# Kernel optimization log

Measured on AMD Instinct MI355X. Metric: run time of the kernel, lower is better.

Reference implementation:

```python
import jax, jax.numpy as jnp
import numpy as np


def setup_inputs() -> dict:
    key = jax.random.key(0)
    k1, k2, k3, k4 = jax.random.split(key, 4)
    B, T, C, H, W = 16, 8, 1024, 14, 14
    x = jax.random.normal(k1, (B * T, C, H, W), dtype=jnp.float32)
    # learned spectral filter, stored as real/imag pairs: [T, H, W, C//2+1, 2]
    wfilt = jax.random.normal(k2, (T, H, W, C // 2 + 1, 2), dtype=jnp.float32) * 0.02
    # 1x1x1 Conv3d over channels -> plain [out, in] matrix + bias
    conv_w = jax.random.normal(k3, (C, C), dtype=jnp.float32) * (1.0 / np.sqrt(C))
    conv_b = jax.random.normal(k4, (C,), dtype=jnp.float32) * 0.01
    return {"x": x, "wfilt": wfilt, "conv_w": conv_w, "conv_b": conv_b, "n_segments": T}


def reference(x, wfilt, conv_w, conv_b, n_segments):
    bt, c, h, w = x.shape
    t = n_segments
    b = bt // t
    x5 = x.reshape(b, t, c, h, w)
    # move channels last: [b, t, h, w, c]
    d = jnp.transpose(x5, (0, 1, 3, 4, 2))
    # rFFT along channel axis, ortho norm
    f = jnp.fft.rfft(d, axis=4, norm="ortho")  # [b, t, h, w, c//2+1]
    wc = jax.lax.complex(wfilt[..., 0], wfilt[..., 1])  # [t, h, w, c//2+1]
    f = f * wc  # broadcast over batch
    d = jnp.fft.irfft(f, n=c, axis=4, norm="ortho")  # [b, t, h, w, c]
    d = jnp.transpose(d, (0, 1, 4, 2, 3))  # [b, t, c, h, w]
    # enhancement: 1x1x1 Conv3d over channels + exact GELU
    e = jnp.einsum("btchw,oc->btohw", d, conv_w) + conv_b[None, None, :, None, None]
    e = jax.nn.gelu(e, approximate=False)
    return (x5 + e).reshape(bt, c, h, w)
```

## Files before the change

### kernel.cpp

```cpp
#include <hip/hip_runtime.h>
#include <hip/hip_bf16.h>
#include <math.h>

typedef short short8 __attribute__((ext_vector_type(8)));
typedef float f32x4 __attribute__((ext_vector_type(4)));

#define BTN   128
#define HWN   196
#define CCH   1024
#define NPIX  (BTN * HWN)
#define BTSTR (CCH * HWN)

#define WS_D  0
#define WS_BW 51380224

__device__ __forceinline__ float2 cadd(float2 a, float2 b) { return make_float2(a.x + b.x, a.y + b.y); }
__device__ __forceinline__ float2 csub(float2 a, float2 b) { return make_float2(a.x - b.x, a.y - b.y); }
__device__ __forceinline__ float2 cmulf(float2 a, float2 b) {
  return make_float2(a.x * b.x - a.y * b.y, a.x * b.y + a.y * b.x);
}
__device__ __forceinline__ float2 cmulc(float2 a, float2 b) {
  return make_float2(a.x * b.x + a.y * b.y, a.y * b.x - a.x * b.y);
}
__device__ __forceinline__ float2 csqr(float2 a) {
  return make_float2(a.x * a.x - a.y * a.y, 2.f * a.x * a.y);
}
__device__ __forceinline__ float2 cneg(float2 a) { return make_float2(-a.x, -a.y); }
__device__ __forceinline__ unsigned short f2bf(float f) {
  unsigned u = __float_as_uint(f);
  unsigned r = (u + 0x7fffu + ((u >> 16) & 1u)) >> 16;
  return (unsigned short)r;
}

__global__ void wcast_kernel(const float* __restrict__ w, unsigned short* __restrict__ o) {
  int i = (blockIdx.x * 256 + threadIdx.x) * 4;
  float4 v = *(const float4*)(w + i);
  uint2 u;
  u.x = (unsigned)f2bf(v.x) | ((unsigned)f2bf(v.y) << 16);
  u.y = (unsigned)f2bf(v.z) | ((unsigned)f2bf(v.w) << 16);
  *(uint2*)(o + i) = u;
}

#define TS 1028

__global__ __launch_bounds__(256) void fft_filter_kernel(
    const float* __restrict__ x, const float* __restrict__ wfilt,
    unsigned short* __restrict__ dmat) {
  __shared__ float tile[8 * TS];
  __shared__ float2 tw10s[257];
  int tid = threadIdx.x;
  int l = tid & 63, w = tid >> 6;

  for (int i = tid; i < 257; i += 256) {
    float s, c;
    __sincosf(-6.283185307179586f * (float)i / 1024.0f, &s, &c);
    tw10s[i] = make_float2(c, s);
  }

  int blk = (blockIdx.x & 7) * 392 + (blockIdx.x >> 3);
  int p_base = blk * 8;

  {
    int g = tid & 1, chb = tid >> 1;
    int p = p_base + 4 * g;
    int bt = p / HWN, hw = p - bt * HWN;
    const float* src = x + (size_t)bt * BTSTR + hw;
    float* rowb = tile + (4 * g) * TS;
#pragma unroll
    for (int it = 0; it < 8; ++it) {
      int c = chb + 128 * it;
      float4 v = *(const float4*)(src + (size_t)c * HWN);
      float* b = rowb + c;
      b[0 * TS] = v.x; b[1 * TS] = v.y; b[2 * TS] = v.z; b[3 * TS] = v.w;
    }
  }
  __syncthreads();

  const float H = 0.70710678118654752f;
  float2 Wl;
  { float s, c; __sincosf(-6.283185307179586f * (float)l / 512.0f, &s, &c); Wl = make_float2(c, s); }
  float2 W2l = csqr(Wl), W4l = csqr(W2l);
  float2 W2li = make_float2(W2l.y, -W2l.x);
  float2 T01 = cmulf(Wl, make_float2(H, -H));
  float2 T02 = make_float2(Wl.y, -Wl.x);
  float2 T03 = cmulf(Wl, make_float2(-H, -H));
  float2 t3 = csqr(W4l); if (l & 32) t3 = cneg(t3);
  float2 t4 = csqr(t3);  if (l & 16) t4 = cneg(t4);
  float2 t5 = csqr(t4);  if (l & 8)  t5 = cneg(t5);
  float2 t6 = csqr(t5);  if (l & 4)  t6 = cneg(t6);
  float2 t7 = csqr(t6);  if (l & 2)  t7 = cneg(t7);

#pragma unroll 1
  for (int pp = 0; pp < 2; ++pp) {
    int px = w * 2 + pp;
    int p = p_base + px;
    int bt = p / HWN, hw = p - bt * HWN;
    float2* zrow = (float2*)(tile + px * TS);

    float2 zr[8];
#pragma unroll
    for (int r = 0; r < 8; ++r) zr[r] = zrow[l + 64 * r];

    {
      float2 T0[4] = {Wl, T01, T02, T03};
#pragma unroll
      for (int r = 0; r < 4; ++r) {
        float2 a = zr[r], b = zr[r + 4];
        zr[r] = cadd(a, b);
        zr[r + 4] = cmulf(csub(a, b), T0[r]);
      }
    }
#pragma unroll
    for (int h = 0; h < 2; ++h) {
      int b0 = h * 4;
      float2 a = zr[b0], b = zr[b0 + 2];
      zr[b0] = cadd(a, b); zr[b0 + 2] = cmulf(csub(a, b), W2l);
      a = zr[b0 + 1]; b = zr[b0 + 3];
      zr[b0 + 1] = cadd(a, b); zr[b0 + 3] = cmulf(csub(a, b), W2li);
    }
#pragma unroll
    for (int r = 0; r < 8; r += 2) {
      float2 a = zr[r], b = zr[r + 1];
      zr[r] = cadd(a, b); zr[r + 1] = cmulf(csub(a, b), W4l);
    }
    {
      float2 tws[6] = {t3, t4, t5, t6, t7, make_float2(1.f, 0.f)};
      int masks[6] = {32, 16, 8, 4, 2, 1};
#pragma unroll
      for (int s = 0; s < 6; ++s) {
        int m = masks[s];
        bool up = (l & m) != 0;
        float2 te = up ? tws[s] : make_float2(1.f, 0.f);
#pragma unroll
        for (int r = 0; r < 8; ++r) {
          float2 v = zr[r];
          float2 o = make_float2(__shfl_xor(v.x, m, 64), __shfl_xor(v.y, m, 64));
          float2 d = up ? csub(o, v) : cadd(v, o);
          zr[r] = cmulf(d, te);
        }
      }
    }

#pragma unroll
    for (int r = 0; r < 8; ++r) zrow[l + 64 * r] = zr[r];
    {
      float2* z = zrow;
      const float* wf = wfilt + (size_t)((bt & 7) * HWN + hw) * 1026;
      const float sc = 1.0f / 512.0f;
#pragma unroll
      for (int i = 0; i < 4; ++i) {
        int f = 64 * i + l;
        if (f == 0) {
          float2 z0 = z[0];
          float X0 = z0.x + z0.y, X512 = z0.x - z0.y;
          float Y0 = X0 * wf[0] * sc;
          float Y512 = X512 * wf[1024] * sc;
          z[0] = make_float2(0.5f * (Y0 + Y512), 0.5f * (Y0 - Y512));
          float2 z2 = z[1];
          float2 X256 = make_float2(z2.x, -z2.y);
          float2 Y = cmulf(X256, make_float2(wf[512], wf[513]));
          z[1] = make_float2(Y.x * sc, -Y.y * sc);
        } else {
          int g = 512 - f;
          int pf = (int)(__brev((unsigned)f) >> 23);
          int pg = (int)(__brev((unsigned)g) >> 23);
          float2 Zf = z[pf], Zg = z[pg];
          float2 A = make_float2(0.5f * (Zf.x + Zg.x), 0.5f * (Zf.y - Zg.y));
          float2 B = make_float2(0.5f * (Zf.y + Zg.y), -0.5f * (Zf.x - Zg.x));
          float2 Wf = tw10s[f];
          float2 WB = cmulf(Wf, B);
          float2 Xf = make_float2(A.x + WB.x, A.y + WB.y);
          float2 Xg = make_float2(A.x - WB.x, -(A.y - WB.y));
          float2 Yf = cmulf(Xf, make_float2(wf[2 * f], wf[2 * f + 1]));
          float2 Yg = cmulf(Xg, make_float2(wf[2 * g], wf[2 * g + 1]));
          Yf.x *= sc; Yf.y *= sc; Yg.x *= sc; Yg.y *= sc;
          float2 Ap = make_float2(0.5f * (Yf.x + Yg.x), 0.5f * (Yf.y - Yg.y));
          float2 T  = make_float2(0.5f * (Yf.x - Yg.x), 0.5f * (Yf.y + Yg.y));
          float2 Bp = cmulf(make_float2(Wf.x, -Wf.y), T);
          z[pf] = make_float2(Ap.x - Bp.y, Ap.y + Bp.x);
          z[pg] = make_float2(Ap.x + Bp.y, Bp.x - Ap.y);
        }
      }
    }
#pragma unroll
    for (int r = 0; r < 8; ++r) zr[r] = zrow[l + 64 * r];

    {
      float2 tws[6] = {make_float2(1.f, 0.f), t7, t6, t5, t4, t3};
      int masks[6] = {1, 2, 4, 8, 16, 32};
#pragma unroll
      for (int s = 0; s < 6; ++s) {
        int m = masks[s];
        bool up = (l & m) != 0;
        float2 te = up ? make_float2(tws[s].x, -tws[s].y) : make_float2(1.f, 0.f);
#pragma unroll
        for (int r = 0; r < 8; ++r) {
          float2 v = cmulf(zr[r], te);
          float2 o = make_float2(__shfl_xor(v.x, m, 64), __shfl_xor(v.y, m, 64));
          zr[r] = up ? csub(o, v) : cadd(v, o);
        }
      }
    }
#pragma unroll
    for (int r = 0; r < 8; r += 2) {
      float2 v = cmulc(zr[r + 1], W4l);
      float2 a = zr[r];
      zr[r] = cadd(a, v); zr[r + 1] = csub(a, v);
    }
#pragma unroll
    for (int h = 0; h < 2; ++h) {
      int b0 = h * 4;
      float2 v = cmulc(zr[b0 + 2], W2l);
      float2 a = zr[b0];
      zr[b0] = cadd(a, v); zr[b0 + 2] = csub(a, v);
      v = cmulc(zr[b0 + 3], W2li);
      a = zr[b0 + 1];
      zr[b0 + 1] = cadd(a, v); zr[b0 + 3] = csub(a, v);
    }
    {
      float2 T0[4] = {Wl, T01, T02, T03};
#pragma unroll
      for (int r = 0; r < 4; ++r) {
        float2 v = cmulc(zr[r + 4], T0[r]);
        float2 a = zr[r];
        zr[r] = cadd(a, v); zr[r + 4] = csub(a, v);
      }
    }

    unsigned* dst = (unsigned*)(dmat + (size_t)p * CCH);
#pragma unroll
    for (int r = 0; r < 8; ++r) {
      float2 v = zr[r];
      dst[l + 64 * r] = (unsigned)f2bf(v.x) | ((unsigned)f2bf(v.y) << 16);
    }
  }
}

#define GLOAD16(gsrc, ldst)                                                     \
  __builtin_amdgcn_global_load_lds(                                             \
      (const __attribute__((address_space(1))) unsigned int*)(gsrc),            \
      (__attribute__((address_space(3))) unsigned int*)(ldst), 16, 0, 0)

__global__ __launch_bounds__(512) void gemm_gelu_kernel(
    const unsigned short* __restrict__ A,
    const unsigned short* __restrict__ Bw,
    const float* __restrict__ bias,
    const float* __restrict__ x,
    float* __restrict__ out) {
  __shared__ unsigned short SH[16384];
  unsigned short* lA = SH;
  unsigned short* lB = SH + 8192;

  int bid = blockIdx.x;
  int j = (bid & 7) * 196 + (bid >> 3);
  int mt = j >> 3, nt = j & 7;
  int p0 = mt * 128, n0 = nt * 128;

  int tid = threadIdx.x;
  int l = tid & 63, wid = tid >> 6;
  int wr = wid >> 2, wc = wid & 3;
  int lr = l & 15, lg = l >> 4;

  f32x4 acc[2][4];
#pragma unroll
  for (int i = 0; i < 2; ++i)
#pragma unroll
    for (int jj = 0; jj < 4; ++jj) acc[i][jj] = f32x4{0.f, 0.f, 0.f, 0.f};

  int arow = tid >> 2;
  int acg = (tid & 3) ^ ((tid >> 3) & 3);
  const unsigned short* agA = A  + (size_t)(p0 + arow) * CCH + acg * 8;
  const unsigned short* agB = Bw + (size_t)(n0 + arow) * CCH + acg * 8;
  unsigned short* laW = lA + wid * 512;
  unsigned short* lbW = lB + wid * 512;

  int kx = ((lg ^ ((lr >> 1) & 3)) << 3);
  const unsigned short* lAf0 = lA + (wr * 64 + lr) * 32 + kx;
  const unsigned short* lBf0 = lB + (wc * 32 + lr) * 32 + kx;

#define STAGE(buf, kt)                                                          \
  do {                                                                          \
    GLOAD16(agA + (kt) * 32, laW + (buf) * 4096);                               \
    GLOAD16(agB + (kt) * 32, lbW + (buf) * 4096);                               \
  } while (0)

  STAGE(0, 0);
  __builtin_amdgcn_sched_barrier(0);
  asm volatile("s_waitcnt vmcnt(0)" ::: "memory");
  __builtin_amdgcn_s_barrier();
  __builtin_amdgcn_sched_barrier(0);

  int cur = 0;
#pragma unroll 2
  for (int kk = 0; kk < 32; ++kk) {
    STAGE(cur ^ 1, (kk + 1) & 31);
    __builtin_amdgcn_sched_barrier(0);
    asm volatile("s_waitcnt vmcnt(2)" ::: "memory");
    __builtin_amdgcn_s_barrier();
    __builtin_amdgcn_sched_barrier(0);

    short8 af[4], bf[2];
    const unsigned short* lAf = lAf0 + cur * 4096;
    const unsigned short* lBf = lBf0 + cur * 4096;
#pragma unroll
    for (int m = 0; m < 4; ++m) af[m] = *(const short8*)(lAf + m * 512);
#pragma unroll
    for (int n = 0; n < 2; ++n) bf[n] = *(const short8*)(lBf + n * 512);
    __builtin_amdgcn_s_setprio(1);
#pragma unroll
    for (int i = 0; i < 2; ++i)
#pragma unroll
      for (int jj = 0; jj < 4; ++jj)
        acc[i][jj] = __builtin_amdgcn_mfma_f32_16x16x32_bf16(bf[i], af[jj], acc[i][jj], 0, 0, 0);
    __builtin_amdgcn_s_setprio(0);
    __builtin_amdgcn_sched_barrier(0);
    __builtin_amdgcn_s_barrier();
    __builtin_amdgcn_sched_barrier(0);
    cur ^= 1;
  }
#undef STAGE
  asm volatile("s_waitcnt vmcnt(0)" ::: "memory");
  __syncthreads();

  float* tp = (float*)SH + wid * 544;
  int pxb = p0 + wr * 64 + (l & 15) * 4;
  int btE = pxb / HWN, hwE = pxb - btE * HWN;
  size_t ebase = (size_t)btE * BTSTR + hwE;

#pragma unroll
  for (int i = 0; i < 2; ++i) {
#pragma unroll
    for (int rr = 0; rr < 2; ++rr) {
#pragma unroll
      for (int jj = 0; jj < 4; ++jj) {
#pragma unroll
        for (int s = 0; s < 2; ++s)
          tp[(lg * 2 + s) * 68 + jj * 16 + lr] = acc[i][jj][2 * rr + s];
      }
      asm volatile("s_waitcnt lgkmcnt(0)" ::: "memory");
      __builtin_amdgcn_sched_barrier(0);
#pragma unroll
      for (int cb = 0; cb < 8; cb += 4) {
        int ct = cb + (l >> 4);
        f32x4 v4 = *(const f32x4*)(tp + ct * 68 + (l & 15) * 4);
        int ch = n0 + wc * 32 + i * 16 + ((ct >> 1) << 2) + 2 * rr + (ct & 1);
        size_t idx = ebase + (size_t)ch * HWN;
        float4 xv = *(const float4*)(x + idx);
        float bc = bias[ch];
        float4 ov;
        {
          float v0 = v4[0] + bc, v1 = v4[1] + bc, v2 = v4[2] + bc, v3 = v4[3] + bc;
          ov.x = xv.x + 0.5f * v0 * (1.0f + erff(v0 * 0.70710678118654752f));
          ov.y = xv.y + 0.5f * v1 * (1.0f + erff(v1 * 0.70710678118654752f));
          ov.z = xv.z + 0.5f * v2 * (1.0f + erff(v2 * 0.70710678118654752f));
          ov.w = xv.w + 0.5f * v3 * (1.0f + erff(v3 * 0.70710678118654752f));
        }
        *(float4*)(out + idx) = ov;
      }
      __builtin_amdgcn_sched_barrier(0);
    }
  }
}

extern "C" void kernel_launch(void* const* d_in, const int* in_sizes, int n_in,
                              void* d_out, int out_size, void* d_ws, size_t ws_size,
                              hipStream_t stream) {
  const float* x      = (const float*)d_in[0];
  const float* wfilt  = (const float*)d_in[1];
  const float* conv_w = (const float*)d_in[2];
  const float* conv_b = (const float*)d_in[3];
  char* ws = (char*)d_ws;
  unsigned short* dmat = (unsigned short*)(ws + WS_D);
  unsigned short* bw   = (unsigned short*)(ws + WS_BW);
  float* out           = (float*)d_out;

  wcast_kernel<<<1024, 256, 0, stream>>>(conv_w, bw);
  fft_filter_kernel<<<3136, 256, 0, stream>>>(x, wfilt, dmat);
  gemm_gelu_kernel<<<1568, 512, 0, stream>>>(dmat, bw, conv_b, x, out);
}
```

Baseline: 192.7 us.

## Interleave two pixel FFTs per wave and pad LDS rows for bit-reversed access

```diff
diff --git a/kernel.cpp b/kernel.cpp
--- a/kernel.cpp
+++ b/kernel.cpp
@@ -41,7 +41,7 @@
   *(uint2*)(o + i) = u;
 }
 
-#define TS 1028
+#define TS 1088
 
 __global__ __launch_bounds__(256) void fft_filter_kernel(
     const float* __restrict__ x, const float* __restrict__ wfilt,
@@ -90,84 +90,113 @@
   float2 t6 = csqr(t5);  if (l & 4)  t6 = cneg(t6);
   float2 t7 = csqr(t6);  if (l & 2)  t7 = cneg(t7);
 
-#pragma unroll 1
-  for (int pp = 0; pp < 2; ++pp) {
-    int px = w * 2 + pp;
-    int p = p_base + px;
-    int bt = p / HWN, hw = p - bt * HWN;
-    float2* zrow = (float2*)(tile + px * TS);
-
-    float2 zr[8];
-#pragma unroll
-    for (int r = 0; r < 8; ++r) zr[r] = zrow[l + 64 * r];
-
-    {
-      float2 T0[4] = {Wl, T01, T02, T03};
+  int pA = p_base + 2 * w, pB = pA + 1;
+  int btA = pA / HWN, hwA = pA - btA * HWN;
+  int btB = pB / HWN, hwB = pB - btB * HWN;
+  float2* rowA = (float2*)(tile + (2 * w) * TS);
+  float2* rowB = (float2*)(tile + (2 * w + 1) * TS);
+
+  float2 z[2][8];
+#pragma unroll
+  for (int r = 0; r < 8; ++r) { z[0][r] = rowA[l + 64 * r]; z[1][r] = rowB[l + 64 * r]; }
+
+  {
+    float2 T0[4] = {Wl, T01, T02, T03};
+#pragma unroll
+    for (int q = 0; q < 2; ++q)
 #pragma unroll
       for (int r = 0; r < 4; ++r) {
-        float2 a = zr[r], b = zr[r + 4];
-        zr[r] = cadd(a, b);
-        zr[r + 4] = cmulf(csub(a, b), T0[r]);
+        float2 a = z[q][r], b = z[q][r + 4];
+        z[q][r] = cadd(a, b);
+        z[q][r + 4] = cmulf(csub(a, b), T0[r]);
       }
-    }
+  }
+#pragma unroll
+  for (int q = 0; q < 2; ++q)
 #pragma unroll
     for (int h = 0; h < 2; ++h) {
       int b0 = h * 4;
-      float2 a = zr[b0], b = zr[b0 + 2];
-      zr[b0] = cadd(a, b); zr[b0 + 2] = cmulf(csub(a, b), W2l);
-      a = zr[b0 + 1]; b = zr[b0 + 3];
-      zr[b0 + 1] = cadd(a, b); zr[b0 + 3] = cmulf(csub(a, b), W2li);
-    }
+      float2 a = z[q][b0], b = z[q][b0 + 2];
+      z[q][b0] = cadd(a, b); z[q][b0 + 2] = cmulf(csub(a, b), W2l);
+      a = z[q][b0 + 1]; b = z[q][b0 + 3];
+      z[q][b0 + 1] = cadd(a, b); z[q][b0 + 3] = cmulf(csub(a, b), W2li);
+    }
+#pragma unroll
+  for (int q = 0; q < 2; ++q)
 #pragma unroll
     for (int r = 0; r < 8; r += 2) {
-      float2 a = zr[r], b = zr[r + 1];
-      zr[r] = cadd(a, b); zr[r + 1] = cmulf(csub(a, b), W4l);
-    }
-    {
-      float2 tws[6] = {t3, t4, t5, t6, t7, make_float2(1.f, 0.f)};
-      int masks[6] = {32, 16, 8, 4, 2, 1};
-#pragma unroll
-      for (int s = 0; s < 6; ++s) {
-        int m = masks[s];
-        bool up = (l & m) != 0;
-        float2 te = up ? tws[s] : make_float2(1.f, 0.f);
-#pragma unroll
-        for (int r = 0; r < 8; ++r) {
-          float2 v = zr[r];
+      float2 a = z[q][r], b = z[q][r + 1];
+      z[q][r] = cadd(a, b); z[q][r + 1] = cmulf(csub(a, b), W4l);
+    }
+  {
+    float2 tws[6] = {t3, t4, t5, t6, t7, make_float2(1.f, 0.f)};
+    int masks[6] = {32, 16, 8, 4, 2, 1};
+#pragma unroll
+    for (int s = 0; s < 6; ++s) {
+      int m = masks[s];
+      bool up = (l & m) != 0;
+      float2 te = up ? tws[s] : make_float2(1.f, 0.f);
+#pragma unroll
+      for (int r = 0; r < 8; ++r)
+#pragma unroll
+        for (int q = 0; q < 2; ++q) {
+          float2 v = z[q][r];
           float2 o = make_float2(__shfl_xor(v.x, m, 64), __shfl_xor(v.y, m, 64));
           float2 d = up ? csub(o, v) : cadd(v, o);
-          zr[r] = cmulf(d, te);
-        }
-      }
-    }
-
-#pragma unroll
-    for (int r = 0; r < 8; ++r) zrow[l + 64 * r] = zr[r];
-    {
-      float2* z = zrow;
-      const float* wf = wfilt + (size_t)((bt & 7) * HWN + hw) * 1026;
-      const float sc = 1.0f / 512.0f;
-#pragma unroll
-      for (int i = 0; i < 4; ++i) {
-        int f = 64 * i + l;
-        if (f == 0) {
-          float2 z0 = z[0];
+          z[q][r] = cmulf(d, te);
+        }
+    }
+  }
+
+#pragma unroll
+  for (int r = 0; r < 8; ++r) {
+    int pidx = l + (l >> 4) + 68 * r;
+    rowA[pidx] = z[0][r]; rowB[pidx] = z[1][r];
+  }
+  {
+    const float* wfA = wfilt + (size_t)((btA & 7) * HWN + hwA) * 1026;
+    const float* wfB = wfilt + (size_t)((btB & 7) * HWN + hwB) * 1026;
+    const float sc = 1.0f / 512.0f;
+#pragma unroll
+    for (int i = 0; i < 4; ++i) {
+      int f = 64 * i + l;
+      if (f == 0) {
+        {
+          float2 z0 = rowA[0];
           float X0 = z0.x + z0.y, X512 = z0.x - z0.y;
-          float Y0 = X0 * wf[0] * sc;
-          float Y512 = X512 * wf[1024] * sc;
-          z[0] = make_float2(0.5f * (Y0 + Y512), 0.5f * (Y0 - Y512));
-          float2 z2 = z[1];
+          float Y0 = X0 * wfA[0] * sc;
+          float Y512 = X512 * wfA[1024] * sc;
+          rowA[0] = make_float2(0.5f * (Y0 + Y512), 0.5f * (Y0 - Y512));
+          float2 z2 = rowA[1];
           float2 X256 = make_float2(z2.x, -z2.y);
-          float2 Y = cmulf(X256, make_float2(wf[512], wf[513]));
-          z[1] = make_float2(Y.x * sc, -Y.y * sc);
-        } else {
-          int g = 512 - f;
-          int pf = (int)(__brev((unsigned)f) >> 23);
-          int pg = (int)(__brev((unsigned)g) >> 23);
-          float2 Zf = z[pf], Zg = z[pg];
+          float2 Y = cmulf(X256, make_float2(wfA[512], wfA[513]));
+          rowA[1] = make_float2(Y.x * sc, -Y.y * sc);
+        }
+        {
+          float2 z0 = rowB[0];
+          float X0 = z0.x + z0.y, X512 = z0.x - z0.y;
+          float Y0 = X0 * wfB[0] * sc;
+          float Y512 = X512 * wfB[1024] * sc;
+          rowB[0] = make_float2(0.5f * (Y0 + Y512), 0.5f * (Y0 - Y512));
+          float2 z2 = rowB[1];
+          float2 X256 = make_float2(z2.x, -z2.y);
+          float2 Y = cmulf(X256, make_float2(wfB[512], wfB[513]));
+          rowB[1] = make_float2(Y.x * sc, -Y.y * sc);
+        }
+      } else {
+        int g = 512 - f;
+        int pf = (int)(__brev((unsigned)f) >> 23);
+        int pg = (int)(__brev((unsigned)g) >> 23);
+        int pf2 = pf + (pf >> 4), pg2 = pg + (pg >> 4);
+        float2 Wf = tw10s[f];
+        float2 Wfc = make_float2(Wf.x, -Wf.y);
+#pragma unroll
+        for (int q = 0; q < 2; ++q) {
+          float2* zq = q ? rowB : rowA;
+          const float* wf = q ? wfB : wfA;
+          float2 Zf = zq[pf2], Zg = zq[pg2];
           float2 A = make_float2(0.5f * (Zf.x + Zg.x), 0.5f * (Zf.y - Zg.y));
           float2 B = make_float2(0.5f * (Zf.y + Zg.y), -0.5f * (Zf.x - Zg.x));
-          float2 Wf = tw10s[f];
           float2 WB = cmulf(Wf, B);
           float2 Xf = make_float2(A.x + WB.x, A.y + WB.y);
           float2 Xg = make_float2(A.x - WB.x, -(A.y - WB.y));
@@ -176,63 +205,76 @@
           Yf.x *= sc; Yf.y *= sc; Yg.x *= sc; Yg.y *= sc;
           float2 Ap = make_float2(0.5f * (Yf.x + Yg.x), 0.5f * (Yf.y - Yg.y));
           float2 T  = make_float2(0.5f * (Yf.x - Yg.x), 0.5f * (Yf.y + Yg.y));
-          float2 Bp = cmulf(make_float2(Wf.x, -Wf.y), T);
-          z[pf] = make_float2(Ap.x - Bp.y, Ap.y + Bp.x);
-          z[pg] = make_float2(Ap.x + Bp.y, Bp.x - Ap.y);
+          float2 Bp = cmulf(Wfc, T);
+          zq[pf2] = make_float2(Ap.x - Bp.y, Ap.y + Bp.x);
+          zq[pg2] = make_float2(Ap.x + Bp.y, Bp.x - Ap.y);
         }
       }
     }
-#pragma unroll
-    for (int r = 0; r < 8; ++r) zr[r] = zrow[l + 64 * r];
-
-    {
-      float2 tws[6] = {make_float2(1.f, 0.f), t7, t6, t5, t4, t3};
-      int masks[6] = {1, 2, 4, 8, 16, 32};
-#pragma unroll
-      for (int s = 0; s < 6; ++s) {
-        int m = masks[s];
-        bool up = (l & m) != 0;
-        float2 te = up ? make_float2(tws[s].x, -tws[s].y) : make_float2(1.f, 0.f);
-#pragma unroll
-        for (int r = 0; r < 8; ++r) {
-          float2 v = cmulf(zr[r], te);
+  }
+#pragma unroll
+  for (int r = 0; r < 8; ++r) {
+    int pidx = l + (l >> 4) + 68 * r;
+    z[0][r] = rowA[pidx]; z[1][r] = rowB[pidx];
+  }
+
+  {
+    float2 tws[6] = {make_float2(1.f, 0.f), t7, t6, t5, t4, t3};
+    int masks[6] = {1, 2, 4, 8, 16, 32};
+#pragma unroll
+    for (int s = 0; s < 6; ++s) {
+      int m = masks[s];
+      bool up = (l & m) != 0;
+      float2 te = up ? make_float2(tws[s].x, -tws[s].y) : make_float2(1.f, 0.f);
+#pragma unroll
+      for (int r = 0; r < 8; ++r)
+#pragma unroll
+        for (int q = 0; q < 2; ++q) {
+          float2 v = cmulf(z[q][r], te);
           float2 o = make_float2(__shfl_xor(v.x, m, 64), __shfl_xor(v.y, m, 64));
-          zr[r] = up ? csub(o, v) : cadd(v, o);
-        }
-      }
-    }
+          z[q][r] = up ? csub(o, v) : cadd(v, o);
+        }
+    }
+  }
+#pragma unroll
+  for (int q = 0; q < 2; ++q)
 #pragma unroll
     for (int r = 0; r < 8; r += 2) {
-      float2 v = cmulc(zr[r + 1], W4l);
-      float2 a = zr[r];
-      zr[r] = cadd(a, v); zr[r + 1] = csub(a, v);
-    }
+      float2 v = cmulc(z[q][r + 1], W4l);
+      float2 a = z[q][r];
+      z[q][r] = cadd(a, v); z[q][r + 1] = csub(a, v);
+    }
+#pragma unroll
+  for (int q = 0; q < 2; ++q)
 #pragma unroll
     for (int h = 0; h < 2; ++h) {
       int b0 = h * 4;
-      float2 v = cmulc(zr[b0 + 2], W2l);
-      float2 a = zr[b0];
-      zr[b0] = cadd(a, v); zr[b0 + 2] = csub(a, v);
-      v = cmulc(zr[b0 + 3], W2li);
-      a = zr[b0 + 1];
-      zr[b0 + 1] = cadd(a, v); zr[b0 + 3] = csub(a, v);
-    }
-    {
-      float2 T0[4] = {Wl, T01, T02, T03};
+      float2 v = cmulc(z[q][b0 + 2], W2l);
+      float2 a = z[q][b0];
+      z[q][b0] = cadd(a, v); z[q][b0 + 2] = csub(a, v);
+      v = cmulc(z[q][b0 + 3], W2li);
+      a = z[q][b0 + 1];
+      z[q][b0 + 1] = cadd(a, v); z[q][b0 + 3] = csub(a, v);
+    }
+  {
+    float2 T0[4] = {Wl, T01, T02, T03};
+#pragma unroll
+    for (int q = 0; q < 2; ++q)
 #pragma unroll
       for (int r = 0; r < 4; ++r) {
-        float2 v = cmulc(zr[r + 4], T0[r]);
-        float2 a = zr[r];
-        zr[r] = cadd(a, v); zr[r + 4] = csub(a, v);
+        float2 v = cmulc(z[q][r + 4], T0[r]);
+        float2 a = z[q][r];
+        z[q][r] = cadd(a, v); z[q][r + 4] = csub(a, v);
       }
-    }
-
-    unsigned* dst = (unsigned*)(dmat + (size_t)p * CCH);
-#pragma unroll
-    for (int r = 0; r < 8; ++r) {
-      float2 v = zr[r];
-      dst[l + 64 * r] = (unsigned)f2bf(v.x) | ((unsigned)f2bf(v.y) << 16);
-    }
+  }
+
+  unsigned* dstA = (unsigned*)(dmat + (size_t)pA * CCH);
+  unsigned* dstB = (unsigned*)(dmat + (size_t)pB * CCH);
+#pragma unroll
+  for (int r = 0; r < 8; ++r) {
+    float2 vA = z[0][r], vB = z[1][r];
+    dstA[l + 64 * r] = (unsigned)f2bf(vA.x) | ((unsigned)f2bf(vA.y) << 16);
+    dstB[l + 64 * r] = (unsigned)f2bf(vB.x) | ((unsigned)f2bf(vB.y) << 16);
   }
 }
 
```

After: 168.4 us, median of 2. -12.6%, faster.
